# Optimization experiments

Hardware: AMD Instinct MI355X
Metric: run time of the kernel (lower is better)

Reference implementation:

```python
import jax, jax.numpy as jnp
import numpy as np

B, S, F, H, L = 4096, 512, 8, 10, 2


def setup_inputs() -> dict:
    key = jax.random.key(0)
    ks = jax.random.split(key, 12)
    bound = 1.0 / np.sqrt(H)  # PyTorch LSTM/Linear init scale
    u = lambda k, shape: jax.random.uniform(k, shape, jnp.float32, -bound, bound)
    return {
        "input_tensor": jax.random.normal(ks[0], (B, S, F), jnp.float32),
        "hidden": jnp.zeros((L, B, H), jnp.float32),
        "cell": jnp.zeros((L, B, H), jnp.float32),
        # layer 0 (input size F), layer 1 (input size H); gate order i,f,g,o
        "W_ih0": u(ks[1], (4 * H, F)), "W_hh0": u(ks[2], (4 * H, H)),
        "b_ih0": u(ks[3], (4 * H,)),   "b_hh0": u(ks[4], (4 * H,)),
        "W_ih1": u(ks[5], (4 * H, H)), "W_hh1": u(ks[6], (4 * H, H)),
        "b_ih1": u(ks[7], (4 * H,)),   "b_hh1": u(ks[8], (4 * H,)),
        "W_fc": u(ks[9], (1, H)),      "b_fc": u(ks[10], (1,)),
    }


def _lstm_layer(x_sbf, h0, c0, W_ih, W_hh, b_ih, b_hh):
    # x_sbf: [S, B, Fin]; h0,c0: [B, H]. Returns hs [S,B,H], (hT, cT).
    b = b_ih + b_hh

    def step(carry, x):
        h, c = carry
        gates = x @ W_ih.T + h @ W_hh.T + b  # [B, 4H]
        i, f, g, o = jnp.split(gates, 4, axis=-1)
        c = jax.nn.sigmoid(f) * c + jax.nn.sigmoid(i) * jnp.tanh(g)
        h = jax.nn.sigmoid(o) * jnp.tanh(c)
        return (h, c), h

    (hT, cT), hs = jax.lax.scan(step, (h0, c0), x_sbf)
    return hs, hT, cT


def reference(input_tensor, hidden, cell,
              W_ih0, W_hh0, b_ih0, b_hh0,
              W_ih1, W_hh1, b_ih1, b_hh1,
              W_fc, b_fc):
    x = jnp.transpose(input_tensor, (1, 0, 2))  # [S, B, F]
    hs0, h0T, c0T = _lstm_layer(x, hidden[0], cell[0], W_ih0, W_hh0, b_ih0, b_hh0)
    hs1, h1T, c1T = _lstm_layer(hs0, hidden[1], cell[1], W_ih1, W_hh1, b_ih1, b_hh1)
    out = hs1[-1]                      # last timestep, [B, H]
    out_regression = out @ W_fc.T + b_fc  # [B, 1]
    hidden_out = jnp.stack([h0T, h1T])
    cell_out = jnp.stack([c0T, c1T])
    return out_regression, hidden_out, cell_out
```

## Files before the change

kernel.cpp:

```cpp
#include <hip/hip_runtime.h>


typedef __fp16 v2h __attribute__((ext_vector_type(2)));
typedef __fp16 v8h __attribute__((ext_vector_type(8)));
struct h4 { v2h a, b, c, d; };

#define L2E 1.4426950408889634f

__device__ __forceinline__ v2h pkh(float a, float b) {
    return __builtin_amdgcn_cvt_pkrtz(a, b);
}
__device__ __forceinline__ float bpermf(int baddr, float v) {
    int r = __builtin_amdgcn_ds_bpermute(baddr, __builtin_bit_cast(int, v));
    return __builtin_bit_cast(float, r);
}

#define SIGM(a)  __builtin_amdgcn_rcpf(1.0f + __builtin_amdgcn_exp2f(-(a)))
#define TANHP(a) fmaf(-2.0f, __builtin_amdgcn_rcpf(1.0f + __builtin_amdgcn_exp2f(a)), 1.0f)
#define DOT2(acc, w, v) (acc) = __builtin_amdgcn_fdot2((w), (v), (acc), false)

#define READROW(PTR, H)                                                      \
    { v8h w0_ = *(const v8h*)(PTR);                                          \
      v2h w1_ = *(const v2h*)((PTR) + 8);                                    \
      h4 q_ = __builtin_bit_cast(h4, w0_);                                   \
      H[0]=q_.a; H[1]=q_.b; H[2]=q_.c; H[3]=q_.d; H[4]=w1_; }

__global__ __launch_bounds__(128, 2)
void lstm2_r15(const float* __restrict__ x,
               const float* __restrict__ hid,
               const float* __restrict__ cel,
               const float* __restrict__ Wih0, const float* __restrict__ Whh0,
               const float* __restrict__ bih0, const float* __restrict__ bhh0,
               const float* __restrict__ Wih1, const float* __restrict__ Whh1,
               const float* __restrict__ bih1, const float* __restrict__ bhh1,
               const float* __restrict__ Wfc,  const float* __restrict__ bfc,
               float* __restrict__ out)
{
    __shared__ __attribute__((aligned(16))) __fp16 h0buf[16][3][24];
    __shared__ __attribute__((aligned(16))) __fp16 h1buf[3][24];
    __shared__ float fcb[3][10];

    const int tid  = threadIdx.x;
    const int lane = tid & 63;
    const int uwid = __builtin_amdgcn_readfirstlane(tid >> 6);
    int grp = lane / 20;
    int l20 = lane - grp * 20;
    if (lane >= 60) { grp = 2; l20 = 19; }
    const int  ju       = (l20 < 10) ? l20 : l20 - 10;
    const bool unitlane = (l20 < 10);
    const int  eIw = grp;
    const int  e   = blockIdx.x * 3 + eIw;
    const int  ec  = (e < 4095) ? e : 4095;
    const int  baddr = ((l20 < 10) ? (lane + 10) : lane) * 4;

    const float alpha2 = unitlane ? 2.0f : 1.0f;
    const float beta2  = unitlane ? -1.0f : 0.0f;
    const float scB    = unitlane ? 2.0f * L2E : L2E;
    const int   rA = l20, rB = 20 + l20;

    if (uwid == 0) {
        v2h wxA[4], wxB[4], whA[5], whB[5];
        #pragma unroll
        for (int k = 0; k < 4; ++k) {
            wxA[k] = pkh(Wih0[rA*8+2*k]*L2E, Wih0[rA*8+2*k+1]*L2E);
            wxB[k] = pkh(Wih0[rB*8+2*k]*scB, Wih0[rB*8+2*k+1]*scB);
        }
        #pragma unroll
        for (int k = 0; k < 5; ++k) {
            whA[k] = pkh(Whh0[rA*10+2*k]*L2E, Whh0[rA*10+2*k+1]*L2E);
            whB[k] = pkh(Whh0[rB*10+2*k]*scB, Whh0[rB*10+2*k+1]*scB);
        }
        const float bA = (bih0[rA] + bhh0[rA]) * L2E;
        const float bB = (bih0[rB] + bhh0[rB]) * scB;

        v2h hv[5];
        #pragma unroll
        for (int k = 0; k < 5; ++k) hv[k] = pkh(hid[ec*10+2*k], hid[ec*10+2*k+1]);
        float cc = cel[ec * 10 + ju];
        float hj = 0.0f;

        __fp16* const wbase = &h0buf[0][eIw][0];
        __fp16* const wlane = wbase + l20;

        const float4* __restrict__ xp = reinterpret_cast<const float4*>(x + (size_t)ec * 4096);
        float4 xb0[2], xb1[2], xb2[2], xb3[2];
        xb0[0]=xp[0]; xb0[1]=xp[1];  xb1[0]=xp[2]; xb1[1]=xp[3];
        xb2[0]=xp[4]; xb2[1]=xp[5];  xb3[0]=xp[6]; xb3[1]=xp[7];

        float axA[2], axB[2];
        {
            v2h x0=pkh(xb0[0].x,xb0[0].y), x1=pkh(xb0[0].z,xb0[0].w);
            v2h x2=pkh(xb0[1].x,xb0[1].y), x3=pkh(xb0[1].z,xb0[1].w);
            xb0[0]=xp[8]; xb0[1]=xp[9];
            float nA=bA, nB=bB;
            DOT2(nA,wxA[0],x0); DOT2(nB,wxB[0],x0);
            DOT2(nA,wxA[1],x1); DOT2(nB,wxB[1],x1);
            DOT2(nA,wxA[2],x2); DOT2(nB,wxB[2],x2);
            DOT2(nA,wxA[3],x3); DOT2(nB,wxB[3],x3);
            axA[0]=nA; axB[0]=nB;
        }

#define L0STEP(S, XB, TN, PC, PN)                                            \
        {                                                                    \
            v2h x0=pkh(XB[0].x,XB[0].y), x1=pkh(XB[0].z,XB[0].w);            \
            v2h x2=pkh(XB[1].x,XB[1].y), x3=pkh(XB[1].z,XB[1].w);            \
            { int tn=(TN)>511?511:(TN); XB[0]=xp[2*tn]; XB[1]=xp[2*tn+1]; }  \
            float nA=bA, nB=bB;                                              \
            DOT2(nA,wxA[0],x0); DOT2(nB,wxB[0],x0);                          \
            DOT2(nA,wxA[1],x1); DOT2(nB,wxB[1],x1);                          \
            DOT2(nA,wxA[2],x2); DOT2(nB,wxB[2],x2);                          \
            DOT2(nA,wxA[3],x3); DOT2(nB,wxB[3],x3);                          \
            axA[PN]=nA; axB[PN]=nB;                                          \
            float aA=axA[PC], aB=axB[PC];                                    \
            DOT2(aA,whA[0],hv[0]); DOT2(aB,whB[0],hv[0]);                    \
            DOT2(aA,whA[1],hv[1]); DOT2(aB,whB[1],hv[1]);                    \
            DOT2(aA,whA[2],hv[2]); DOT2(aB,whB[2],hv[2]);                    \
            DOT2(aA,whA[3],hv[3]); DOT2(aB,whB[3],hv[3]);                    \
            DOT2(aA,whA[4],hv[4]); DOT2(aB,whB[4],hv[4]);                    \
            float r1 = SIGM(aA);                                             \
            float r2 = __builtin_amdgcn_rcpf(1.0f + __builtin_amdgcn_exp2f(-aB)); \
            float act2 = fmaf(alpha2, r2, beta2);                            \
            float ig = r1 * act2;                                            \
            float sf = bpermf(baddr, r1);                                    \
            float so = bpermf(baddr, act2);                                  \
            cc = fmaf(sf, cc, ig);                                           \
            hj = so * TANHP((2.0f*L2E) * cc);                                \
            wlane[(S)*72] = (__fp16)hj;                                      \
            READROW(wbase + (S)*72, hv)                                      \
        }

        for (int it = 0; it < 32; ++it) {
            const int tb = 16 * it;
            L0STEP(0,  xb1, tb+5,  0, 1)
            L0STEP(1,  xb2, tb+6,  1, 0)
            L0STEP(2,  xb3, tb+7,  0, 1)
            L0STEP(3,  xb0, tb+8,  1, 0)
            L0STEP(4,  xb1, tb+9,  0, 1)
            L0STEP(5,  xb2, tb+10, 1, 0)
            L0STEP(6,  xb3, tb+11, 0, 1)
            L0STEP(7,  xb0, tb+12, 1, 0)
            __syncthreads();
            L0STEP(8,  xb1, tb+13, 0, 1)
            L0STEP(9,  xb2, tb+14, 1, 0)
            L0STEP(10, xb3, tb+15, 0, 1)
            L0STEP(11, xb0, tb+16, 1, 0)
            L0STEP(12, xb1, tb+17, 0, 1)
            L0STEP(13, xb2, tb+18, 1, 0)
            L0STEP(14, xb3, tb+19, 0, 1)
            L0STEP(15, xb0, tb+20, 1, 0)
            __syncthreads();
        }
#undef L0STEP

        __syncthreads();
        if (unitlane && e < 4096) {
            out[4096          + e * 10 + ju] = hj;
            out[4096 + 81920  + e * 10 + ju] = cc;
        }

    } else {
        v2h wiA[5], wiB[5], whA[5], whB[5];
        #pragma unroll
        for (int k = 0; k < 5; ++k) {
            wiA[k] = pkh(Wih1[rA*10+2*k]*L2E, Wih1[rA*10+2*k+1]*L2E);
            wiB[k] = pkh(Wih1[rB*10+2*k]*scB, Wih1[rB*10+2*k+1]*scB);
            whA[k] = pkh(Whh1[rA*10+2*k]*L2E, Whh1[rA*10+2*k+1]*L2E);
            whB[k] = pkh(Whh1[rB*10+2*k]*scB, Whh1[rB*10+2*k+1]*scB);
        }
        const float bA = (bih1[rA] + bhh1[rA]) * L2E;
        const float bB = (bih1[rB] + bhh1[rB]) * scB;
        const float wfc = Wfc[ju];

        v2h hv[5];
        #pragma unroll
        for (int k = 0; k < 5; ++k) hv[k] = pkh(hid[40960+ec*10+2*k], hid[40960+ec*10+2*k+1]);
        float cc = cel[40960 + ec * 10 + ju];
        float hj = 0.0f;

        const __fp16* const rbase = &h0buf[0][eIw][0];
        __fp16* const h1w  = &h1buf[eIw][0];
        __fp16* const h1wl = h1w + l20;

        float axA[2], axB[2];

#define L1PRE(S, P)                                                          \
        {                                                                    \
            v2h pr[5];                                                       \
            READROW(rbase + (S)*72, pr)                                      \
            float nA=bA, nB=bB;                                              \
            DOT2(nA,wiA[0],pr[0]); DOT2(nB,wiB[0],pr[0]);                    \
            DOT2(nA,wiA[1],pr[1]); DOT2(nB,wiB[1],pr[1]);                    \
            DOT2(nA,wiA[2],pr[2]); DOT2(nB,wiB[2],pr[2]);                    \
            DOT2(nA,wiA[3],pr[3]); DOT2(nB,wiB[3],pr[3]);                    \
            DOT2(nA,wiA[4],pr[4]); DOT2(nB,wiB[4],pr[4]);                    \
            axA[P]=nA; axB[P]=nB;                                            \
        }

#define L1CORE(PC)                                                           \
        {                                                                    \
            float aA=axA[PC], aB=axB[PC];                                    \
            DOT2(aA,whA[0],hv[0]); DOT2(aB,whB[0],hv[0]);                    \
            DOT2(aA,whA[1],hv[1]); DOT2(aB,whB[1],hv[1]);                    \
            DOT2(aA,whA[2],hv[2]); DOT2(aB,whB[2],hv[2]);                    \
            DOT2(aA,whA[3],hv[3]); DOT2(aB,whB[3],hv[3]);                    \
            DOT2(aA,whA[4],hv[4]); DOT2(aB,whB[4],hv[4]);                    \
            float r1 = SIGM(aA);                                             \
            float r2 = __builtin_amdgcn_rcpf(1.0f + __builtin_amdgcn_exp2f(-aB)); \
            float act2 = fmaf(alpha2, r2, beta2);                            \
            float ig = r1 * act2;                                            \
            float sf = bpermf(baddr, r1);                                    \
            float so = bpermf(baddr, act2);                                  \
            cc = fmaf(sf, cc, ig);                                           \
            hj = so * TANHP((2.0f*L2E) * cc);                                \
            h1wl[0] = (__fp16)hj;                                            \
            READROW(h1w, hv)                                                 \
        }

        for (int it = 0; it < 32; ++it) {
            __syncthreads();
            L1PRE(0, 0)
            L1PRE(1, 1) L1CORE(0)
            L1PRE(2, 0) L1CORE(1)
            L1PRE(3, 1) L1CORE(0)
            L1PRE(4, 0) L1CORE(1)
            L1PRE(5, 1) L1CORE(0)
            L1PRE(6, 0) L1CORE(1)
            L1PRE(7, 1) L1CORE(0)
            L1CORE(1)
            __syncthreads();
            L1PRE(8, 0)
            L1PRE(9,  1) L1CORE(0)
            L1PRE(10, 0) L1CORE(1)
            L1PRE(11, 1) L1CORE(0)
            L1PRE(12, 0) L1CORE(1)
            L1PRE(13, 1) L1CORE(0)
            L1PRE(14, 0) L1CORE(1)
            L1PRE(15, 1) L1CORE(0)
            L1CORE(1)
        }
#undef L1PRE
#undef L1CORE

        if (unitlane) fcb[eIw][ju] = hj * wfc;
        __syncthreads();
        if (l20 == 0 && e < 4096) {
            float p = bfc[0];
            #pragma unroll
            for (int k = 0; k < 10; ++k) p += fcb[eIw][k];
            out[e] = p;
        }
        if (unitlane && e < 4096) {
            out[4096 + 40960  + e * 10 + ju] = hj;
            out[4096 + 122880 + e * 10 + ju] = cc;
        }
    }
}

extern "C" void kernel_launch(void* const* d_in, const int* in_sizes, int n_in,
                              void* d_out, int out_size, void* d_ws, size_t ws_size,
                              hipStream_t stream) {
    const float* x    = (const float*)d_in[0];
    const float* hid  = (const float*)d_in[1];
    const float* cel  = (const float*)d_in[2];
    const float* Wih0 = (const float*)d_in[3];
    const float* Whh0 = (const float*)d_in[4];
    const float* bih0 = (const float*)d_in[5];
    const float* bhh0 = (const float*)d_in[6];
    const float* Wih1 = (const float*)d_in[7];
    const float* Whh1 = (const float*)d_in[8];
    const float* bih1 = (const float*)d_in[9];
    const float* bhh1 = (const float*)d_in[10];
    const float* Wfc  = (const float*)d_in[11];
    const float* bfc  = (const float*)d_in[12];

    hipLaunchKernelGGL(lstm2_r15, dim3(1366), dim3(128), 0, stream,
                       x, hid, cel, Wih0, Whh0, bih0, bhh0,
                       Wih1, Whh1, bih1, bhh1, Wfc, bfc,
                       (float*)d_out);
}
```

Measured before the change: 193.5 us.

## Pack two batch elements per wave across four-wave blocks

Each block now runs 256 threads: two layer-0 waves and two layer-1 waves, each wave holding two batch elements (40 active lanes) instead of three. The grid becomes 1024 blocks, which divides the batch exactly, so the clamped index and bounds checks are gone. The x-prefetch pointer now advances incrementally, and the last iteration is peeled to skip out-of-range loads. This changes waves per element and occupancy: fewer elements per wave means more waves overall and 24 idle lanes per wave, in exchange for removing the 4-lane tail waste and using a larger block for barrier sharing.

Result: slower. 199.9 us (+3.3%).

```diff
diff --git a/kernel.cpp b/kernel.cpp
--- a/kernel.cpp
+++ b/kernel.cpp
@@ -25,8 +25,8 @@
       h4 q_ = __builtin_bit_cast(h4, w0_);                                   \
       H[0]=q_.a; H[1]=q_.b; H[2]=q_.c; H[3]=q_.d; H[4]=w1_; }
 
-__global__ __launch_bounds__(128, 2)
-void lstm2_r15(const float* __restrict__ x,
+__global__ __launch_bounds__(256, 4)
+void lstm2_r16(const float* __restrict__ x,
                const float* __restrict__ hid,
                const float* __restrict__ cel,
                const float* __restrict__ Wih0, const float* __restrict__ Whh0,
@@ -36,29 +36,28 @@
                const float* __restrict__ Wfc,  const float* __restrict__ bfc,
                float* __restrict__ out)
 {
-    __shared__ __attribute__((aligned(16))) __fp16 h0buf[16][3][24];
-    __shared__ __attribute__((aligned(16))) __fp16 h1buf[3][24];
-    __shared__ float fcb[3][10];
+    __shared__ __attribute__((aligned(16))) __fp16 h0buf[16][4][24];
+    __shared__ __attribute__((aligned(16))) __fp16 h1buf[4][24];
+    __shared__ float fcb[4][10];
 
     const int tid  = threadIdx.x;
     const int lane = tid & 63;
     const int uwid = __builtin_amdgcn_readfirstlane(tid >> 6);
     int grp = lane / 20;
     int l20 = lane - grp * 20;
-    if (lane >= 60) { grp = 2; l20 = 19; }
+    if (lane >= 40) { grp = 1; l20 = 19; }
     const int  ju       = (l20 < 10) ? l20 : l20 - 10;
-    const bool unitlane = (l20 < 10);
-    const int  eIw = grp;
-    const int  e   = blockIdx.x * 3 + eIw;
-    const int  ec  = (e < 4095) ? e : 4095;
+    const bool unitlane = (l20 < 10) && (lane < 40);
+    const int  eIw = (uwid & 1) * 2 + grp;
+    const int  e   = blockIdx.x * 4 + eIw;
     const int  baddr = ((l20 < 10) ? (lane + 10) : lane) * 4;
 
-    const float alpha2 = unitlane ? 2.0f : 1.0f;
-    const float beta2  = unitlane ? -1.0f : 0.0f;
-    const float scB    = unitlane ? 2.0f * L2E : L2E;
+    const float alpha2 = (l20 < 10) ? 2.0f : 1.0f;
+    const float beta2  = (l20 < 10) ? -1.0f : 0.0f;
+    const float scB    = (l20 < 10) ? 2.0f * L2E : L2E;
     const int   rA = l20, rB = 20 + l20;
 
-    if (uwid == 0) {
+    if (uwid < 2) {
         v2h wxA[4], wxB[4], whA[5], whB[5];
         #pragma unroll
         for (int k = 0; k < 4; ++k) {
@@ -75,23 +74,23 @@
 
         v2h hv[5];
         #pragma unroll
-        for (int k = 0; k < 5; ++k) hv[k] = pkh(hid[ec*10+2*k], hid[ec*10+2*k+1]);
-        float cc = cel[ec * 10 + ju];
+        for (int k = 0; k < 5; ++k) hv[k] = pkh(hid[e*10+2*k], hid[e*10+2*k+1]);
+        float cc = cel[e * 10 + ju];
         float hj = 0.0f;
 
         __fp16* const wbase = &h0buf[0][eIw][0];
         __fp16* const wlane = wbase + l20;
 
-        const float4* __restrict__ xp = reinterpret_cast<const float4*>(x + (size_t)ec * 4096);
+        const float4* __restrict__ xp4 = reinterpret_cast<const float4*>(x + (size_t)e * 4096);
         float4 xb0[2], xb1[2], xb2[2], xb3[2];
-        xb0[0]=xp[0]; xb0[1]=xp[1];  xb1[0]=xp[2]; xb1[1]=xp[3];
-        xb2[0]=xp[4]; xb2[1]=xp[5];  xb3[0]=xp[6]; xb3[1]=xp[7];
+        xb0[0]=xp4[0]; xb0[1]=xp4[1];  xb1[0]=xp4[2]; xb1[1]=xp4[3];
+        xb2[0]=xp4[4]; xb2[1]=xp4[5];  xb3[0]=xp4[6]; xb3[1]=xp4[7];
 
         float axA[2], axB[2];
         {
             v2h x0=pkh(xb0[0].x,xb0[0].y), x1=pkh(xb0[0].z,xb0[0].w);
             v2h x2=pkh(xb0[1].x,xb0[1].y), x3=pkh(xb0[1].z,xb0[1].w);
-            xb0[0]=xp[8]; xb0[1]=xp[9];
+            xb0[0]=xp4[8]; xb0[1]=xp4[9];
             float nA=bA, nB=bB;
             DOT2(nA,wxA[0],x0); DOT2(nB,wxB[0],x0);
             DOT2(nA,wxA[1],x1); DOT2(nB,wxB[1],x1);
@@ -100,11 +99,11 @@
             axA[0]=nA; axB[0]=nB;
         }
 
-#define L0STEP(S, XB, TN, PC, PN)                                            \
+#define L0STEP(S, XB, DOREF, PC, PN)                                         \
         {                                                                    \
             v2h x0=pkh(XB[0].x,XB[0].y), x1=pkh(XB[0].z,XB[0].w);            \
             v2h x2=pkh(XB[1].x,XB[1].y), x3=pkh(XB[1].z,XB[1].w);            \
-            { int tn=(TN)>511?511:(TN); XB[0]=xp[2*tn]; XB[1]=xp[2*tn+1]; }  \
+            if (DOREF) { XB[0]=xr[2*((S)+5)]; XB[1]=xr[2*((S)+5)+1]; }       \
             float nA=bA, nB=bB;                                              \
             DOT2(nA,wxA[0],x0); DOT2(nB,wxB[0],x0);                          \
             DOT2(nA,wxA[1],x1); DOT2(nB,wxB[1],x1);                          \
@@ -125,35 +124,54 @@
             float so = bpermf(baddr, act2);                                  \
             cc = fmaf(sf, cc, ig);                                           \
             hj = so * TANHP((2.0f*L2E) * cc);                                \
-            wlane[(S)*72] = (__fp16)hj;                                      \
-            READROW(wbase + (S)*72, hv)                                      \
-        }
-
-        for (int it = 0; it < 32; ++it) {
-            const int tb = 16 * it;
-            L0STEP(0,  xb1, tb+5,  0, 1)
-            L0STEP(1,  xb2, tb+6,  1, 0)
-            L0STEP(2,  xb3, tb+7,  0, 1)
-            L0STEP(3,  xb0, tb+8,  1, 0)
-            L0STEP(4,  xb1, tb+9,  0, 1)
-            L0STEP(5,  xb2, tb+10, 1, 0)
-            L0STEP(6,  xb3, tb+11, 0, 1)
-            L0STEP(7,  xb0, tb+12, 1, 0)
-            __syncthreads();
-            L0STEP(8,  xb1, tb+13, 0, 1)
-            L0STEP(9,  xb2, tb+14, 1, 0)
-            L0STEP(10, xb3, tb+15, 0, 1)
-            L0STEP(11, xb0, tb+16, 1, 0)
-            L0STEP(12, xb1, tb+17, 0, 1)
-            L0STEP(13, xb2, tb+18, 1, 0)
-            L0STEP(14, xb3, tb+19, 0, 1)
-            L0STEP(15, xb0, tb+20, 1, 0)
-            __syncthreads();
-        }
+            wlane[(S)*96] = (__fp16)hj;                                      \
+            READROW(wbase + (S)*96, hv)                                      \
+        }
+
+        const float4* __restrict__ xr = xp4;
+        for (int it = 0; it < 31; ++it) {
+            L0STEP(0,  xb1, 1, 0, 1)
+            L0STEP(1,  xb2, 1, 1, 0)
+            L0STEP(2,  xb3, 1, 0, 1)
+            L0STEP(3,  xb0, 1, 1, 0)
+            L0STEP(4,  xb1, 1, 0, 1)
+            L0STEP(5,  xb2, 1, 1, 0)
+            L0STEP(6,  xb3, 1, 0, 1)
+            L0STEP(7,  xb0, 1, 1, 0)
+            __syncthreads();
+            L0STEP(8,  xb1, 1, 0, 1)
+            L0STEP(9,  xb2, 1, 1, 0)
+            L0STEP(10, xb3, 1, 0, 1)
+            L0STEP(11, xb0, 1, 1, 0)
+            L0STEP(12, xb1, 1, 0, 1)
+            L0STEP(13, xb2, 1, 1, 0)
+            L0STEP(14, xb3, 1, 0, 1)
+            L0STEP(15, xb0, 1, 1, 0)
+            __syncthreads();
+            xr += 32;
+        }
+        L0STEP(0,  xb1, 1, 0, 1)
+        L0STEP(1,  xb2, 1, 1, 0)
+        L0STEP(2,  xb3, 1, 0, 1)
+        L0STEP(3,  xb0, 1, 1, 0)
+        L0STEP(4,  xb1, 1, 0, 1)
+        L0STEP(5,  xb2, 1, 1, 0)
+        L0STEP(6,  xb3, 1, 0, 1)
+        L0STEP(7,  xb0, 1, 1, 0)
+        __syncthreads();
+        L0STEP(8,  xb1, 1, 0, 1)
+        L0STEP(9,  xb2, 1, 1, 0)
+        L0STEP(10, xb3, 1, 0, 1)
+        L0STEP(11, xb0, 0, 1, 0)
+        L0STEP(12, xb1, 0, 0, 1)
+        L0STEP(13, xb2, 0, 1, 0)
+        L0STEP(14, xb3, 0, 0, 1)
+        L0STEP(15, xb0, 0, 1, 0)
+        __syncthreads();
 #undef L0STEP
 
         __syncthreads();
-        if (unitlane && e < 4096) {
+        if (unitlane) {
             out[4096          + e * 10 + ju] = hj;
             out[4096 + 81920  + e * 10 + ju] = cc;
         }
@@ -173,8 +191,8 @@
 
         v2h hv[5];
         #pragma unroll
-        for (int k = 0; k < 5; ++k) hv[k] = pkh(hid[40960+ec*10+2*k], hid[40960+ec*10+2*k+1]);
-        float cc = cel[40960 + ec * 10 + ju];
+        for (int k = 0; k < 5; ++k) hv[k] = pkh(hid[40960+e*10+2*k], hid[40960+e*10+2*k+1]);
+        float cc = cel[40960 + e * 10 + ju];
         float hj = 0.0f;
 
         const __fp16* const rbase = &h0buf[0][eIw][0];
@@ -186,7 +204,7 @@
 #define L1PRE(S, P)                                                          \
         {                                                                    \
             v2h pr[5];                                                       \
-            READROW(rbase + (S)*72, pr)                                      \
+            READROW(rbase + (S)*96, pr)                                      \
             float nA=bA, nB=bB;                                              \
             DOT2(nA,wiA[0],pr[0]); DOT2(nB,wiB[0],pr[0]);                    \
             DOT2(nA,wiA[1],pr[1]); DOT2(nB,wiB[1],pr[1]);                    \
@@ -243,13 +261,13 @@
 
         if (unitlane) fcb[eIw][ju] = hj * wfc;
         __syncthreads();
-        if (l20 == 0 && e < 4096) {
+        if (l20 == 0 && lane < 40) {
             float p = bfc[0];
             #pragma unroll
             for (int k = 0; k < 10; ++k) p += fcb[eIw][k];
             out[e] = p;
         }
-        if (unitlane && e < 4096) {
+        if (unitlane) {
             out[4096 + 40960  + e * 10 + ju] = hj;
             out[4096 + 122880 + e * 10 + ju] = cc;
         }
@@ -273,7 +291,7 @@
     const float* Wfc  = (const float*)d_in[11];
     const float* bfc  = (const float*)d_in[12];
 
-    hipLaunchKernelGGL(lstm2_r15, dim3(1366), dim3(128), 0, stream,
+    hipLaunchKernelGGL(lstm2_r16, dim3(1024), dim3(256), 0, stream,
                        x, hid, cel, Wih0, Whh0, bih0, bhh0,
                        Wih1, Whh1, bih1, bhh1, Wfc, bfc,
                        (float*)d_out);
```
